# Kernel optimization log

Measured on AMD Instinct MI355X. Metric: run time of the kernel, lower is better.

The kernel has to match this reference:

```python
import jax, jax.numpy as jnp
import numpy as np
import math

N, M, S, D = 256, 512, 128, 512  # num_vids, num_music, num_segments, embed_dim


def layer_norm(x, g, b, eps=1e-5):
    mu = jnp.mean(x, axis=-1, keepdims=True)
    var = jnp.mean(jnp.square(x - mu), axis=-1, keepdims=True)
    return (x - mu) * jax.lax.rsqrt(var + eps) * g + b


def setup_inputs() -> dict:
    key = jax.random.key(0)
    ks = jax.random.split(key, 16)
    s = 0.02
    return {
        "video_embeds": jax.random.normal(ks[0], (N, D), jnp.float32),
        "music_embeds": jax.random.normal(ks[1], (M, S, D), jnp.float32),
        "music_mask": jnp.ones((M, S), jnp.int32),
        "ln1_g": jnp.ones((D,), jnp.float32), "ln1_b": jnp.zeros((D,), jnp.float32),
        "Wq": jax.random.normal(ks[2], (D, D), jnp.float32) * s, "bq": jnp.zeros((D,), jnp.float32),
        "Wk": jax.random.normal(ks[3], (D, D), jnp.float32) * s, "bk": jnp.zeros((D,), jnp.float32),
        "Wv": jax.random.normal(ks[4], (D, D), jnp.float32) * s, "bv": jnp.zeros((D,), jnp.float32),
        "Wo": jax.random.normal(ks[5], (D, D), jnp.float32) * s, "bo": jnp.zeros((D,), jnp.float32),
        "Wl": jax.random.normal(ks[6], (D, D), jnp.float32) * s, "bl": jnp.zeros((D,), jnp.float32),
        "ln2_g": jnp.ones((D,), jnp.float32), "ln2_b": jnp.zeros((D,), jnp.float32),
        "ln3_g": jnp.ones((D,), jnp.float32), "ln3_b": jnp.zeros((D,), jnp.float32),
    }


def reference(video_embeds, music_embeds, music_mask,
              ln1_g, ln1_b, Wq, bq, Wk, bk, Wv, bv, Wo, bo, Wl, bl,
              ln2_g, ln2_b, ln3_g, ln3_b):
    d = video_embeds.shape[-1]
    # layer_norm1 applied to both streams
    v_ln = layer_norm(video_embeds, ln1_g, ln1_b)           # (N, D)
    m_ln = layer_norm(music_embeds, ln1_g, ln1_b)           # (M, S, D)
    # single-head cross-attention (MultiHeadedAttention_mask, num_heads=1)
    q = v_ln @ Wq.T + bq                                    # (N, D)
    k = m_ln @ Wk.T + bk                                    # (M, S, D)
    v = m_ln @ Wv.T + bv                                    # (M, S, D)
    logits = jnp.einsum('nd,msd->mns', q, k) / math.sqrt(d)  # (M, N, S)
    logits = jnp.where(music_mask[:, None, :] == 0, -jnp.inf, logits)
    weights = jax.nn.softmax(logits, axis=-1)               # softmax over segments
    attn = jnp.einsum('mns,msd->mnd', weights, v)           # (M, N, D)
    o = attn @ Wo.T + bo                                    # (M, N, D)
    # layer_norm2 -> linear -> residual (dropout is identity in eval) -> layer_norm3
    o = layer_norm(o, ln2_g, ln2_b)
    lin = o @ Wl.T + bl
    out = layer_norm(o + lin, ln3_g, ln3_b)
    return out
```

## Files before the change

### kernel.cpp

```cpp
#include <hip/hip_runtime.h>

typedef __attribute__((ext_vector_type(8))) short short8;
typedef __attribute__((ext_vector_type(4))) float f32x4;
typedef __attribute__((ext_vector_type(4))) unsigned short u16x4;

__device__ __forceinline__ unsigned short f2bf(float f){
  unsigned int u = __builtin_bit_cast(unsigned int, f);
  u = (u + 0x7FFFu + ((u >> 16) & 1u)) >> 16;
  return (unsigned short)u;
}
__device__ __forceinline__ float bf2f(unsigned short h){
  unsigned int u = ((unsigned int)h) << 16;
  return __builtin_bit_cast(float, u);
}
__device__ __forceinline__ f32x4 mfma16(short8 a, short8 b, f32x4 c){
  return __builtin_amdgcn_mfma_f32_16x16x32_bf16(a, b, c, 0, 0, 0);
}
__device__ __forceinline__ void gload16(const void* g, void* l){
  __builtin_amdgcn_global_load_lds((const __attribute__((address_space(1))) void*)g,
                                   (__attribute__((address_space(3))) void*)l, 16, 0, 0);
}

__global__ __launch_bounds__(256) void cvt2_f32_bf16(const float* __restrict__ s0,
                                                     unsigned short* __restrict__ d0,
                                                     const float* __restrict__ s1,
                                                     unsigned short* __restrict__ d1){
  const int half = blockIdx.x >> 8;
  const float* src = half ? s1 : s0;
  unsigned short* dst = half ? d1 : d0;
  int i = ((blockIdx.x & 255) * 256 + threadIdx.x) * 4;
  float4 v = *(const float4*)(src + i);
  u16x4 o = { f2bf(v.x), f2bf(v.y), f2bf(v.z), f2bf(v.w) };
  *(u16x4*)(dst + i) = o;
}

__global__ __launch_bounds__(256) void copy_bf(const unsigned short* __restrict__ src,
                                               unsigned short* __restrict__ dst){
  int i = (blockIdx.x * 256 + threadIdx.x) * 8;
  *(short8*)(dst + i) = *(const short8*)(src + i);
}

__global__ __launch_bounds__(256) void ln_rows(const float* __restrict__ x,
                                               const float* __restrict__ g,
                                               const float* __restrict__ b,
                                               unsigned short* __restrict__ y,
                                               int nrows){
  const int wid = threadIdx.x >> 6, lane = threadIdx.x & 63;
  const int row = blockIdx.x * 4 + wid;
  if (row >= nrows) return;
  const float* xr = x + (long)row * 512;
  float4 v0 = *(const float4*)(xr + lane * 4);
  float4 v1 = *(const float4*)(xr + 256 + lane * 4);
  float s  = v0.x + v0.y + v0.z + v0.w + v1.x + v1.y + v1.z + v1.w;
  float s2 = v0.x*v0.x + v0.y*v0.y + v0.z*v0.z + v0.w*v0.w
           + v1.x*v1.x + v1.y*v1.y + v1.z*v1.z + v1.w*v1.w;
  #pragma unroll
  for (int m = 1; m < 64; m <<= 1){ s += __shfl_xor(s, m); s2 += __shfl_xor(s2, m); }
  const float mu = s * (1.f/512.f);
  const float rstd = rsqrtf(s2 * (1.f/512.f) - mu*mu + 1e-5f);
  float4 g0 = *(const float4*)(g + lane*4), g1 = *(const float4*)(g + 256 + lane*4);
  float4 b0 = *(const float4*)(b + lane*4), b1 = *(const float4*)(b + 256 + lane*4);
  u16x4 o0 = { f2bf((v0.x-mu)*rstd*g0.x + b0.x), f2bf((v0.y-mu)*rstd*g0.y + b0.y),
               f2bf((v0.z-mu)*rstd*g0.z + b0.z), f2bf((v0.w-mu)*rstd*g0.w + b0.w) };
  u16x4 o1 = { f2bf((v1.x-mu)*rstd*g1.x + b1.x), f2bf((v1.y-mu)*rstd*g1.y + b1.y),
               f2bf((v1.z-mu)*rstd*g1.z + b1.z), f2bf((v1.w-mu)*rstd*g1.w + b1.w) };
  *(u16x4*)(y + (long)row * 512 + lane * 4) = o0;
  *(u16x4*)(y + (long)row * 512 + 256 + lane * 4) = o1;
}

__global__ __launch_bounds__(256) void ln_weight_prep(
    const float* __restrict__ Wl, const float* __restrict__ g2,
    const float* __restrict__ b2, const float* __restrict__ bl,
    const float* __restrict__ bo,
    unsigned short* __restrict__ wlp, float* __restrict__ u,
    float* __restrict__ v, float* __restrict__ bias_cat){
  const int wid = threadIdx.x >> 6, lane = threadIdx.x & 63;
  const int n = blockIdx.x * 4 + wid;
  const float* row = Wl + (long)n * 512;
  float su = 0.f, sv = 0.f, sc = 0.f;
  #pragma unroll
  for (int h = 0; h < 2; ++h){
    const int c0 = h * 256 + lane * 4;
    float4 w  = *(const float4*)(row + c0);
    float4 gg = *(const float4*)(g2 + c0);
    float4 bb = *(const float4*)(b2 + c0);
    float4 oo = *(const float4*)(bo + c0);
    float4 wp = { w.x*gg.x, w.y*gg.y, w.z*gg.z, w.w*gg.w };
    su += wp.x + wp.y + wp.z + wp.w;
    sv += w.x*bb.x + w.y*bb.y + w.z*bb.z + w.w*bb.w;
    sc += wp.x*oo.x + wp.y*oo.y + wp.z*oo.z + wp.w*oo.w;
    u16x4 o = { f2bf(wp.x), f2bf(wp.y), f2bf(wp.z), f2bf(wp.w) };
    *(u16x4*)(wlp + (long)n * 512 + c0) = o;
  }
  #pragma unroll
  for (int m = 1; m < 64; m <<= 1){
    su += __shfl_xor(su, m); sv += __shfl_xor(sv, m); sc += __shfl_xor(sc, m);
  }
  if (lane == 0){
    u[n] = su;
    v[n] = sv + bl[n];
    bias_cat[n] = bo[n];
    bias_cat[512 + n] = sc;
  }
}

__global__ __launch_bounds__(256) void cvb_add(const unsigned short* __restrict__ Bc,
                                               const float* __restrict__ bv,
                                               float* __restrict__ bias_cat){
  const int wid = threadIdx.x >> 6, lane = threadIdx.x & 63;
  const int n = blockIdx.x * 4 + wid;
  const unsigned short* row = Bc + (long)n * 512;
  short8 a = *(const short8*)(row + lane * 8);
  float s = 0.f;
  #pragma unroll
  for (int j = 0; j < 8; ++j) s += bf2f((unsigned short)a[j]) * bv[lane*8 + j];
  #pragma unroll
  for (int m = 1; m < 64; m <<= 1) s += __shfl_xor(s, m);
  if (lane == 0) bias_cat[n] += s;
}

__global__ __launch_bounds__(256) void transpose3_bf(
    const float* __restrict__ s0, unsigned short* __restrict__ d0,
    const float* __restrict__ s1, unsigned short* __restrict__ d1,
    const float* __restrict__ s2, unsigned short* __restrict__ d2){
  __shared__ float tile[64][65];
  const float* src = (blockIdx.z == 0) ? s0 : (blockIdx.z == 1) ? s1 : s2;
  unsigned short* dst = (blockIdx.z == 0) ? d0 : (blockIdx.z == 1) ? d1 : d2;
  const int t = threadIdx.x;
  const int k0 = blockIdx.x * 64, c0 = blockIdx.y * 64;
  const int j = t & 63, i = t >> 6;
  #pragma unroll
  for (int rr = 0; rr < 16; ++rr)
    tile[i + rr*4][j] = src[(long)(c0 + i + rr*4) * 512 + k0 + j];
  __syncthreads();
  #pragma unroll
  for (int rr = 0; rr < 16; ++rr)
    dst[(long)(k0 + i + rr*4) * 512 + c0 + j] = f2bf(tile[j][i + rr*4]);
}

__global__ __launch_bounds__(256) void gemm_bt(const unsigned short* __restrict__ A,
                                               const unsigned short* __restrict__ B,
                                               const float* __restrict__ bias,
                                               unsigned short* __restrict__ out,
                                               int transposed){
  __shared__ unsigned short At[128][40];
  __shared__ unsigned short Bt[128][40];
  const int t = threadIdx.x, lane = t & 63, wid = t >> 6;
  const int l15 = lane & 15, l4 = lane >> 4;
  const int wr = wid >> 1, wc = wid & 1;
  const int rowBase = blockIdx.y * 128;
  const int colBase = blockIdx.x * 128;
  f32x4 zero = {0.f, 0.f, 0.f, 0.f};
  f32x4 acc[4][4];
  #pragma unroll
  for (int i = 0; i < 4; ++i)
    #pragma unroll
    for (int j = 0; j < 4; ++j) acc[i][j] = zero;
  const int sr = t >> 1, sh = (t & 1) * 16;
  for (int ks = 0; ks < 16; ++ks){
    const int k0 = ks * 32;
    const unsigned short* sa = A + (long)(rowBase + sr) * 512 + k0 + sh;
    *(short8*)&At[sr][sh]     = *(const short8*)sa;
    *(short8*)&At[sr][sh + 8] = *(const short8*)(sa + 8);
    const unsigned short* sb = B + (long)(colBase + sr) * 512 + k0 + sh;
    *(short8*)&Bt[sr][sh]     = *(const short8*)sb;
    *(short8*)&Bt[sr][sh + 8] = *(const short8*)(sb + 8);
    __syncthreads();
    short8 af[4], bfv[4];
    #pragma unroll
    for (int i = 0; i < 4; ++i) af[i]  = *(const short8*)&At[wr*64 + i*16 + l15][l4*8];
    #pragma unroll
    for (int i = 0; i < 4; ++i) bfv[i] = *(const short8*)&Bt[wc*64 + i*16 + l15][l4*8];
    #pragma unroll
    for (int i = 0; i < 4; ++i)
      #pragma unroll
      for (int j = 0; j < 4; ++j)
        acc[i][j] = mfma16(af[i], bfv[j], acc[i][j]);
    __syncthreads();
  }
  #pragma unroll
  for (int i = 0; i < 4; ++i){
    const int r0 = rowBase + wr*64 + i*16 + l4*4;
    #pragma unroll
    for (int j = 0; j < 4; ++j){
      const int c = colBase + wc*64 + j*16 + l15;
      const float bb = bias ? bias[c] : 0.f;
      #pragma unroll
      for (int jr = 0; jr < 4; ++jr){
        const float v = acc[i][j][jr] + bb;
        const long rr = r0 + jr;
        if (!transposed){
          out[rr * 512 + c] = f2bf(v);
        } else {
          const long m = rr >> 7, s = rr & 127;
          out[(m * 512 + c) * 128 + s] = f2bf(v);
        }
      }
    }
  }
}

__global__ __launch_bounds__(256) void vb97(const unsigned short* __restrict__ A,
                                            const unsigned short* __restrict__ B,
                                            unsigned short* __restrict__ vbt,
                                            int m0){
  __shared__ unsigned short A_lds[8192];
  __shared__ unsigned short B_lds[8192];
  const int t = threadIdx.x, lane = t & 63, wid = t >> 6;
  const int l15 = lane & 15, l4 = lane >> 4;
  const int wr = wid >> 1, wc = wid & 1;
  const int b = blockIdx.x;
  const int kk = b >> 3;
  const int colBase = (kk & 7) * 128;
  const long panel = m0 + (b & 7) + 8 * (kk >> 3);
  const long rowBase = panel * 128;
  f32x4 zero = {0.f,0.f,0.f,0.f};
  f32x4 acc[4][4];
  #pragma unroll
  for (int i = 0; i < 4; ++i)
    #pragma unroll
    for (int j = 0; j < 4; ++j) acc[i][j] = zero;
  for (int ks = 0; ks < 8; ++ks){
    const int k0 = ks * 64;
    #pragma unroll
    for (int sub = 0; sub < 2; ++sub){
      #pragma unroll
      for (int h = 0; h < 2; ++h){
        const int p = h*256 + t;
        const int row = p >> 2, g = (p & 3) ^ ((row >> 1) & 3);
        gload16(A + (rowBase + row)*512 + k0 + sub*32 + g*8, A_lds + sub*4096 + p*8);
        gload16(B + (long)(colBase + row)*512 + k0 + sub*32 + g*8, B_lds + sub*4096 + p*8);
      }
    }
    __syncthreads();
    #pragma unroll
    for (int sub = 0; sub < 2; ++sub){
      short8 af[4], bfv[4];
      #pragma unroll
      for (int i = 0; i < 4; ++i){
        const int ra = wr*64 + i*16 + l15;
        af[i]  = *(const short8*)(A_lds + sub*4096 + (ra*4 + (l4 ^ ((ra >> 1) & 3)))*8);
        const int rb = wc*64 + i*16 + l15;
        bfv[i] = *(const short8*)(B_lds + sub*4096 + (rb*4 + (l4 ^ ((rb >> 1) & 3)))*8);
      }
      #pragma unroll
      for (int i = 0; i < 4; ++i)
        #pragma unroll
        for (int j = 0; j < 4; ++j)
          acc[i][j] = mfma16(af[i], bfv[j], acc[i][j]);
    }
    __syncthreads();
  }
  #pragma unroll
  for (int i = 0; i < 4; ++i){
    const int s0 = wr*64 + i*16 + l4*4;
    #pragma unroll
    for (int j = 0; j < 4; ++j){
      const int n = colBase + wc*64 + j*16 + l15;
      #pragma unroll
      for (int jr = 0; jr < 4; ++jr)
        vbt[((long)panel*1024 + n)*128 + s0 + jr] = f2bf(acc[i][j][jr]);
    }
  }
}

__global__ __launch_bounds__(256) void attn_c(const unsigned short* __restrict__ q2,
                                              const unsigned short* __restrict__ mlnb,
                                              int m_mln0,
                                              const unsigned short* __restrict__ vbt,
                                              const int* __restrict__ mask,
                                              unsigned short* __restrict__ C,
                                              int m0){
  __shared__ __align__(16) char smem[81920];
  unsigned short* q_lin = (unsigned short*)smem;
  unsigned short* k_lin = (unsigned short*)(smem + 65536);
  unsigned short (*w_lds)[136] = (unsigned short (*)[136])smem;
  float* red = (float*)(smem + 17408);
  unsigned short* v_lin = (unsigned short*)(smem + 19456);
  const int b = blockIdx.x;
  const int m_local = (b & 7) + 8 * (b >> 5);
  const int qb = (b >> 3) & 3;
  const int m = m0 + m_local;
  const int t = threadIdx.x, lane = t & 63, wid = t >> 6;
  const int l15 = lane & 15, l4 = lane >> 4;
  #pragma unroll
  for (int it = 0; it < 16; ++it){
    const int p = it*256 + t;
    const int row = p >> 6, gp = p & 63;
    const int gsrc = gp ^ (row & 7);
    gload16(q2 + (long)(qb*64 + row)*512 + gsrc*8, q_lin + p*8);
  }
  f32x4 zero = {0.f,0.f,0.f,0.f};
  f32x4 acc[4][2];
  #pragma unroll
  for (int i = 0; i < 4; ++i){ acc[i][0] = zero; acc[i][1] = zero; }
  const unsigned short* kbase = mlnb + (long)(m - m_mln0) * 128 * 512;
  for (int ks = 0; ks < 8; ++ks){
    const int k0 = ks * 64;
    #pragma unroll
    for (int sub = 0; sub < 2; ++sub){
      #pragma unroll
      for (int h = 0; h < 2; ++h){
        const int p = h*256 + t;
        const int row = p >> 2, g = (p & 3) ^ ((row >> 1) & 3);
        gload16(kbase + (long)row*512 + k0 + sub*32 + g*8, k_lin + sub*4096 + p*8);
      }
    }
    __syncthreads();
    #pragma unroll
    for (int sub = 0; sub < 2; ++sub){
      const int kk32 = ks*2 + sub;
      short8 af[4], bfv[2];
      #pragma unroll
      for (int i = 0; i < 4; ++i){
        const int row = i*16 + l15;
        const int gp = (kk32*4 + l4) ^ (l15 & 7);
        af[i] = *(const short8*)(q_lin + (row*64 + gp)*8);
      }
      #pragma unroll
      for (int j = 0; j < 2; ++j){
        const int rb = wid*32 + j*16 + l15;
        bfv[j] = *(const short8*)(k_lin + sub*4096 + (rb*4 + (l4 ^ ((rb >> 1) & 3)))*8);
      }
      #pragma unroll
      for (int i = 0; i < 4; ++i)
        #pragma unroll
        for (int j = 0; j < 2; ++j)
          acc[i][j] = mfma16(af[i], bfv[j], acc[i][j]);
    }
    __syncthreads();
  }
  const float scale = 0.04419417382415922f;
  const int* mrow = mask + m * 128;
  const int mk0 = mrow[wid*32 + l15];
  const int mk1 = mrow[wid*32 + 16 + l15];
  float e[4][2][4], wmax[4][4], wsum[4][4];
  #pragma unroll
  for (int i = 0; i < 4; ++i)
    #pragma unroll
    for (int jr = 0; jr < 4; ++jr){
      float v0 = mk0 ? acc[i][0][jr]*scale : -3.0e38f;
      float v1 = mk1 ? acc[i][1][jr]*scale : -3.0e38f;
      float mx = fmaxf(v0, v1);
      mx = fmaxf(mx, __shfl_xor(mx, 1));
      mx = fmaxf(mx, __shfl_xor(mx, 2));
      mx = fmaxf(mx, __shfl_xor(mx, 4));
      mx = fmaxf(mx, __shfl_xor(mx, 8));
      const float e0 = __expf(v0 - mx), e1 = __expf(v1 - mx);
      float sm = e0 + e1;
      sm += __shfl_xor(sm, 1);
      sm += __shfl_xor(sm, 2);
      sm += __shfl_xor(sm, 4);
      sm += __shfl_xor(sm, 8);
      e[i][0][jr] = e0; e[i][1][jr] = e1;
      wmax[i][jr] = mx; wsum[i][jr] = sm;
    }
  if (l15 == 0){
    #pragma unroll
    for (int i = 0; i < 4; ++i)
      #pragma unroll
      for (int jr = 0; jr < 4; ++jr){
        const int r = i*16 + l4*4 + jr;
        red[r*8 + wid*2]     = wmax[i][jr];
        red[r*8 + wid*2 + 1] = wsum[i][jr];
      }
  }
  __syncthreads();
  #pragma unroll
  for (int i = 0; i < 4; ++i)
    #pragma unroll
    for (int jr = 0; jr < 4; ++jr){
      const int r = i*16 + l4*4 + jr;
      float4 a = *(const float4*)(red + r*8);
      float4 c = *(const float4*)(red + r*8 + 4);
      const float gm = fmaxf(fmaxf(a.x, a.z), fmaxf(c.x, c.z));
      const float gs = a.y*__expf(a.x - gm) + a.w*__expf(a.z - gm)
                     + c.y*__expf(c.x - gm) + c.w*__expf(c.z - gm);
      const float inv = (gs > 0.f) ? (1.f / gs) : 0.f;
      const float sc = __expf(wmax[i][jr] - gm) * inv;
      #pragma unroll
      for (int j = 0; j < 2; ++j)
        w_lds[r][wid*32 + j*16 + l15] = f2bf(e[i][j][jr] * sc);
    }
  const long rowb = (long)m * 256 + qb * 64;
  const unsigned short* vbase = vbt + (long)m * 1024 * 128;
  for (int nb = 0; nb < 8; ++nb){
    __syncthreads();
    #pragma unroll
    for (int it = 0; it < 8; ++it){
      const int p = it*256 + t;
      const int row = p >> 4, g = (p & 15) ^ (row & 7);
      gload16(vbase + (long)(nb*128 + row)*128 + g*8, v_lin + p*8);
    }
    __syncthreads();
    f32x4 pacc[4][2];
    #pragma unroll
    for (int i = 0; i < 4; ++i){ pacc[i][0] = zero; pacc[i][1] = zero; }
    #pragma unroll
    for (int ks2 = 0; ks2 < 4; ++ks2){
      short8 wf[4], vf[2];
      #pragma unroll
      for (int i = 0; i < 4; ++i) wf[i] = *(const short8*)&w_lds[i*16 + l15][ks2*32 + l4*8];
      #pragma unroll
      for (int j = 0; j < 2; ++j){
        const int rv = wid*32 + j*16 + l15;
        vf[j] = *(const short8*)(v_lin + (rv*16 + ((ks2*4 + l4) ^ (rv & 7)))*8);
      }
      #pragma unroll
      for (int i = 0; i < 4; ++i)
        #pragma unroll
        for (int j = 0; j < 2; ++j)
          pacc[i][j] = mfma16(wf[i], vf[j], pacc[i][j]);
    }
    #pragma unroll
    for (int i = 0; i < 4; ++i)
      #pragma unroll
      for (int j = 0; j < 2; ++j)
        #pragma unroll
        for (int jr = 0; jr < 4; ++jr)
          C[(rowb + i*16 + l4*4 + jr) * 1024 + nb*128 + wid*32 + j*16 + l15] =
              f2bf(pacc[i][j][jr]);
  }
}

__global__ __launch_bounds__(256) void ln_epilogue(
    const unsigned short* Cb, float* out,
    const float* __restrict__ bias_cat, const float* __restrict__ u,
    const float* __restrict__ v,
    const float* __restrict__ g2, const float* __restrict__ b2,
    const float* __restrict__ g3, const float* __restrict__ b3){
  const int wid = threadIdx.x >> 6, lane = threadIdx.x & 63;
  const long row = (long)blockIdx.x * 4 + wid;
  const unsigned short* cr = Cb + row * 1024;
  short8 ov = *(const short8*)(cr + lane * 8);
  short8 pv = *(const short8*)(cr + 512 + lane * 8);
  const int n0 = lane * 8;
  float4 bo0 = *(const float4*)(bias_cat + n0);
  float4 bo1 = *(const float4*)(bias_cat + n0 + 4);
  float4 c20 = *(const float4*)(bias_cat + 512 + n0);
  float4 c21 = *(const float4*)(bias_cat + 512 + n0 + 4);
  float o[8], p[8];
  #pragma unroll
  for (int j = 0; j < 4; ++j){
    o[j]   = bf2f((unsigned short)ov[j])   + ((const float*)&bo0)[j];
    o[4+j] = bf2f((unsigned short)ov[4+j]) + ((const float*)&bo1)[j];
    p[j]   = bf2f((unsigned short)pv[j])   + ((const float*)&c20)[j];
    p[4+j] = bf2f((unsigned short)pv[4+j]) + ((const float*)&c21)[j];
  }
  float s = 0.f, s2 = 0.f;
  #pragma unroll
  for (int j = 0; j < 8; ++j){ s += o[j]; s2 += o[j]*o[j]; }
  #pragma unroll
  for (int m = 1; m < 64; m <<= 1){ s += __shfl_xor(s, m); s2 += __shfl_xor(s2, m); }
  const float mu2 = s * (1.f/512.f);
  const float rstd2 = rsqrtf(s2 * (1.f/512.f) - mu2*mu2 + 1e-5f);
  float4 uv0 = *(const float4*)(u + n0), uv1 = *(const float4*)(u + n0 + 4);
  float4 vv0 = *(const float4*)(v + n0), vv1 = *(const float4*)(v + n0 + 4);
  float4 g20v = *(const float4*)(g2 + n0), g21v = *(const float4*)(g2 + n0 + 4);
  float4 b20v = *(const float4*)(b2 + n0), b21v = *(const float4*)(b2 + n0 + 4);
  float y[8];
  #pragma unroll
  for (int j = 0; j < 4; ++j){
    const float lin0 = rstd2 * (p[j]   - mu2 * ((const float*)&uv0)[j]) + ((const float*)&vv0)[j];
    const float lin1 = rstd2 * (p[4+j] - mu2 * ((const float*)&uv1)[j]) + ((const float*)&vv1)[j];
    const float oln0 = (o[j]   - mu2) * rstd2 * ((const float*)&g20v)[j] + ((const float*)&b20v)[j];
    const float oln1 = (o[4+j] - mu2) * rstd2 * ((const float*)&g21v)[j] + ((const float*)&b21v)[j];
    y[j]   = oln0 + lin0;
    y[4+j] = oln1 + lin1;
  }
  float t1 = 0.f, t2 = 0.f;
  #pragma unroll
  for (int j = 0; j < 8; ++j){ t1 += y[j]; t2 += y[j]*y[j]; }
  #pragma unroll
  for (int m = 1; m < 64; m <<= 1){ t1 += __shfl_xor(t1, m); t2 += __shfl_xor(t2, m); }
  const float mu3 = t1 * (1.f/512.f);
  const float rstd3 = rsqrtf(t2 * (1.f/512.f) - mu3*mu3 + 1e-5f);
  float4 g30v = *(const float4*)(g3 + n0), g31v = *(const float4*)(g3 + n0 + 4);
  float4 b30v = *(const float4*)(b3 + n0), b31v = *(const float4*)(b3 + n0 + 4);
  float4 r0, r1;
  #pragma unroll
  for (int j = 0; j < 4; ++j){
    ((float*)&r0)[j] = (y[j]   - mu3) * rstd3 * ((const float*)&g30v)[j] + ((const float*)&b30v)[j];
    ((float*)&r1)[j] = (y[4+j] - mu3) * rstd3 * ((const float*)&g31v)[j] + ((const float*)&b31v)[j];
  }
  *(float4*)(out + row * 512 + n0)     = r0;
  *(float4*)(out + row * 512 + n0 + 4) = r1;
}

extern "C" void kernel_launch(void* const* d_in, const int* in_sizes, int n_in,
                              void* d_out, int out_size, void* d_ws, size_t ws_size,
                              hipStream_t stream){
  const float* video = (const float*)d_in[0];
  const float* music = (const float*)d_in[1];
  const int*   mask  = (const int*)d_in[2];
  const float* ln1g  = (const float*)d_in[3];
  const float* ln1b  = (const float*)d_in[4];
  const float* Wq = (const float*)d_in[5];  const float* bq = (const float*)d_in[6];
  const float* Wk = (const float*)d_in[7];
  const float* Wv = (const float*)d_in[9];  const float* bv = (const float*)d_in[10];
  const float* Wo = (const float*)d_in[11]; const float* bo = (const float*)d_in[12];
  const float* Wl = (const float*)d_in[13]; const float* bl = (const float*)d_in[14];
  const float* g2 = (const float*)d_in[15]; const float* b2 = (const float*)d_in[16];
  const float* g3 = (const float*)d_in[17]; const float* b3 = (const float*)d_in[18];

  char* ob = (char*)d_out;
  unsigned short* mln  = (unsigned short*)(ob + 201326592);
  unsigned short* Cb   = (unsigned short*)ob;
  float* outp = (float*)d_out;

  char* wsb = (char*)d_ws;
  unsigned short* vbt    = (unsigned short*)wsb;
  unsigned short* Wq_bf  = (unsigned short*)(wsb + 134217728);
  unsigned short* Bcat   = Wq_bf + 262144;
  unsigned short* wlp    = Bcat + 524288;
  unsigned short* WoT    = wlp + 262144;
  unsigned short* WkT    = WoT + 262144;
  unsigned short* WvT    = WkT + 262144;
  unsigned short* Wvb    = WvT + 262144;
  unsigned short* q_ws   = Wvb + 524288;
  unsigned short* q2_ws  = q_ws + 131072;
  unsigned short* vln    = q2_ws + 131072;
  unsigned short* mln_cp = vln + 131072;
  float* bias_cat = (float*)(mln_cp + 524288);
  float* u_vec    = bias_cat + 1024;
  float* v_vec    = u_vec + 512;

  cvt2_f32_bf16<<<512, 256, 0, stream>>>(Wq, Wq_bf, Wo, Bcat);
  ln_weight_prep<<<128, 256, 0, stream>>>(Wl, g2, b2, bl, bo, wlp, u_vec, v_vec, bias_cat);
  transpose3_bf<<<dim3(8, 8, 3), 256, 0, stream>>>(Wo, WoT, Wk, WkT, Wv, WvT);
  gemm_bt<<<dim3(4, 4), 256, 0, stream>>>(wlp, WoT, nullptr, Bcat + 262144, 0);
  gemm_bt<<<dim3(4, 8), 256, 0, stream>>>(Bcat, WvT, nullptr, Wvb, 0);
  cvb_add<<<256, 256, 0, stream>>>(Bcat, bv, bias_cat);

  ln_rows<<<16384, 256, 0, stream>>>(music, ln1g, ln1b, mln, 65536);
  ln_rows<<<64,    256, 0, stream>>>(video, ln1g, ln1b, vln, 256);
  gemm_bt<<<dim3(4, 2), 256, 0, stream>>>(vln, Wq_bf, bq, q_ws, 0);
  gemm_bt<<<dim3(4, 2), 256, 0, stream>>>(q_ws, WkT, nullptr, q2_ws, 0);

  const int vm0[5] = {0, 128, 256, 384, 480};
  const int vdm[5] = {128, 128, 128, 96, 32};
  const int am0[5] = {0, 128, 256, 384, 480};
  const int adm[5] = {128, 128, 128, 96, 24};
  for (int cidx = 0; cidx < 5; ++cidx){
    vb97<<<vdm[cidx] * 8, 256, 0, stream>>>(mln, Wvb, vbt, vm0[cidx]);
    const int m0 = am0[cidx], dm = adm[cidx];
    attn_c<<<dm * 4, 256, 0, stream>>>(q2_ws, mln, 0, vbt, mask, Cb, m0);
    ln_epilogue<<<dm * 64, 256, 0, stream>>>(Cb + (long)m0*256*1024,
                                             outp + (long)m0*256*512,
                                             bias_cat, u_vec, v_vec, g2, b2, g3, b3);
  }
  copy_bf<<<256, 256, 0, stream>>>(mln + (long)504*128*512, mln_cp);
  attn_c<<<32, 256, 0, stream>>>(q2_ws, mln_cp, 504, vbt, mask, Cb, 504);
  ln_epilogue<<<512, 256, 0, stream>>>(Cb + (long)504*256*1024,
                                       outp + (long)504*256*512,
                                       bias_cat, u_vec, v_vec, g2, b2, g3, b3);
}
```

Measured before the change: 598.5 us.

## Double-buffer K and V LDS tiles in attention kernel and swizzle weight tile

```diff
diff --git a/kernel.cpp b/kernel.cpp
--- a/kernel.cpp
+++ b/kernel.cpp
@@ -273,10 +273,12 @@
                                               int m0){
   __shared__ __align__(16) char smem[81920];
   unsigned short* q_lin = (unsigned short*)smem;
-  unsigned short* k_lin = (unsigned short*)(smem + 65536);
-  unsigned short (*w_lds)[136] = (unsigned short (*)[136])smem;
-  float* red = (float*)(smem + 17408);
-  unsigned short* v_lin = (unsigned short*)(smem + 19456);
+  unsigned short* k_half0 = (unsigned short*)(smem + 65536);
+  unsigned short* k_half1 = (unsigned short*)(smem + 73728);
+  unsigned short* w_lds = (unsigned short*)smem;
+  unsigned short* v_half0 = (unsigned short*)(smem + 16384);
+  unsigned short* v_half1 = (unsigned short*)(smem + 49152);
+  float* red = (float*)(smem + 49152);
   const int b = blockIdx.x;
   const int m_local = (b & 7) + 8 * (b >> 5);
   const int qb = (b >> 3) & 3;
@@ -295,46 +297,47 @@
   #pragma unroll
   for (int i = 0; i < 4; ++i){ acc[i][0] = zero; acc[i][1] = zero; }
   const unsigned short* kbase = mlnb + (long)(m - m_mln0) * 128 * 512;
-  for (int ks = 0; ks < 8; ++ks){
-    const int k0 = ks * 64;
-    #pragma unroll
-    for (int sub = 0; sub < 2; ++sub){
-      #pragma unroll
-      for (int h = 0; h < 2; ++h){
-        const int p = h*256 + t;
-        const int row = p >> 2, g = (p & 3) ^ ((row >> 1) & 3);
-        gload16(kbase + (long)row*512 + k0 + sub*32 + g*8, k_lin + sub*4096 + p*8);
-      }
-    }
+  #define STAGE_K(ksub, dst)                                                  \
+    do {                                                                      \
+      _Pragma("unroll")                                                       \
+      for (int h2 = 0; h2 < 2; ++h2){                                         \
+        const int p = h2*256 + t;                                             \
+        const int row = p >> 2, g = (p & 3) ^ ((row >> 1) & 3);               \
+        gload16(kbase + (long)row*512 + (ksub)*32 + g*8, (dst) + p*8);        \
+      }                                                                       \
+    } while (0)
+  STAGE_K(0, k_half0);
+  for (int ks = 0; ks < 16; ++ks){
     __syncthreads();
-    #pragma unroll
-    for (int sub = 0; sub < 2; ++sub){
-      const int kk32 = ks*2 + sub;
-      short8 af[4], bfv[2];
-      #pragma unroll
-      for (int i = 0; i < 4; ++i){
-        const int row = i*16 + l15;
-        const int gp = (kk32*4 + l4) ^ (l15 & 7);
-        af[i] = *(const short8*)(q_lin + (row*64 + gp)*8);
-      }
-      #pragma unroll
-      for (int j = 0; j < 2; ++j){
-        const int rb = wid*32 + j*16 + l15;
-        bfv[j] = *(const short8*)(k_lin + sub*4096 + (rb*4 + (l4 ^ ((rb >> 1) & 3)))*8);
-      }
-      #pragma unroll
-      for (int i = 0; i < 4; ++i)
-        #pragma unroll
-        for (int j = 0; j < 2; ++j)
-          acc[i][j] = mfma16(af[i], bfv[j], acc[i][j]);
-    }
-    __syncthreads();
-  }
+    if (ks < 15){
+      if (ks & 1){ STAGE_K(ks + 1, k_half0); } else { STAGE_K(ks + 1, k_half1); }
+    }
+    const unsigned short* kh = (ks & 1) ? k_half1 : k_half0;
+    short8 af[4], bfv[2];
+    #pragma unroll
+    for (int i = 0; i < 4; ++i){
+      const int row = i*16 + l15;
+      const int gp = (ks*4 + l4) ^ (l15 & 7);
+      af[i] = *(const short8*)(q_lin + (row*64 + gp)*8);
+    }
+    #pragma unroll
+    for (int j = 0; j < 2; ++j){
+      const int rb = wid*32 + j*16 + l15;
+      bfv[j] = *(const short8*)(kh + (rb*4 + (l4 ^ ((rb >> 1) & 3)))*8);
+    }
+    #pragma unroll
+    for (int i = 0; i < 4; ++i)
+      #pragma unroll
+      for (int j = 0; j < 2; ++j)
+        acc[i][j] = mfma16(af[i], bfv[j], acc[i][j]);
+  }
+  #undef STAGE_K
+  __syncthreads();
   const float scale = 0.04419417382415922f;
   const int* mrow = mask + m * 128;
   const int mk0 = mrow[wid*32 + l15];
   const int mk1 = mrow[wid*32 + 16 + l15];
-  float e[4][2][4], wmax[4][4], wsum[4][4];
+  float e[4][2][4], wmax[4][4];
   #pragma unroll
   for (int i = 0; i < 4; ++i)
     #pragma unroll
@@ -353,18 +356,13 @@
       sm += __shfl_xor(sm, 4);
       sm += __shfl_xor(sm, 8);
       e[i][0][jr] = e0; e[i][1][jr] = e1;
-      wmax[i][jr] = mx; wsum[i][jr] = sm;
-    }
-  if (l15 == 0){
-    #pragma unroll
-    for (int i = 0; i < 4; ++i)
-      #pragma unroll
-      for (int jr = 0; jr < 4; ++jr){
+      wmax[i][jr] = mx;
+      if (l15 == 0){
         const int r = i*16 + l4*4 + jr;
-        red[r*8 + wid*2]     = wmax[i][jr];
-        red[r*8 + wid*2 + 1] = wsum[i][jr];
-      }
-  }
+        red[r*8 + wid*2]     = mx;
+        red[r*8 + wid*2 + 1] = sm;
+      }
+    }
   __syncthreads();
   #pragma unroll
   for (int i = 0; i < 4; ++i)
@@ -379,20 +377,29 @@
       const float inv = (gs > 0.f) ? (1.f / gs) : 0.f;
       const float sc = __expf(wmax[i][jr] - gm) * inv;
       #pragma unroll
-      for (int j = 0; j < 2; ++j)
-        w_lds[r][wid*32 + j*16 + l15] = f2bf(e[i][j][jr] * sc);
+      for (int j = 0; j < 2; ++j){
+        const int cc = wid*32 + j*16 + l15;
+        w_lds[r*128 + (((cc >> 3) ^ (r & 7)) << 3) + (cc & 7)] = f2bf(e[i][j][jr] * sc);
+      }
     }
   const long rowb = (long)m * 256 + qb * 64;
   const unsigned short* vbase = vbt + (long)m * 1024 * 128;
+  #define STAGE_V(nb, dst)                                                    \
+    do {                                                                      \
+      _Pragma("unroll")                                                       \
+      for (int it = 0; it < 8; ++it){                                         \
+        const int p = it*256 + t;                                             \
+        const int row = p >> 4, g = (p & 15) ^ (row & 7);                     \
+        gload16(vbase + (long)((nb)*128 + row)*128 + g*8, (dst) + p*8);       \
+      }                                                                       \
+    } while (0)
+  STAGE_V(0, v_half0);
   for (int nb = 0; nb < 8; ++nb){
     __syncthreads();
-    #pragma unroll
-    for (int it = 0; it < 8; ++it){
-      const int p = it*256 + t;
-      const int row = p >> 4, g = (p & 15) ^ (row & 7);
-      gload16(vbase + (long)(nb*128 + row)*128 + g*8, v_lin + p*8);
-    }
-    __syncthreads();
+    if (nb < 7){
+      if (nb & 1){ STAGE_V(nb + 1, v_half0); } else { STAGE_V(nb + 1, v_half1); }
+    }
+    const unsigned short* vh = (nb & 1) ? v_half1 : v_half0;
     f32x4 pacc[4][2];
     #pragma unroll
     for (int i = 0; i < 4; ++i){ pacc[i][0] = zero; pacc[i][1] = zero; }
@@ -400,11 +407,15 @@
     for (int ks2 = 0; ks2 < 4; ++ks2){
       short8 wf[4], vf[2];
       #pragma unroll
-      for (int i = 0; i < 4; ++i) wf[i] = *(const short8*)&w_lds[i*16 + l15][ks2*32 + l4*8];
+      for (int i = 0; i < 4; ++i){
+        const int row = i*16 + l15;
+        const int gsw = (ks2*4 + l4) ^ (row & 7);
+        wf[i] = *(const short8*)(w_lds + row*128 + gsw*8);
+      }
       #pragma unroll
       for (int j = 0; j < 2; ++j){
         const int rv = wid*32 + j*16 + l15;
-        vf[j] = *(const short8*)(v_lin + (rv*16 + ((ks2*4 + l4) ^ (rv & 7)))*8);
+        vf[j] = *(const short8*)(vh + (rv*16 + ((ks2*4 + l4) ^ (rv & 7)))*8);
       }
       #pragma unroll
       for (int i = 0; i < 4; ++i)
@@ -421,6 +432,7 @@
           C[(rowb + i*16 + l4*4 + jr) * 1024 + nb*128 + wid*32 + j*16 + l15] =
               f2bf(pacc[i][j][jr]);
   }
+  #undef STAGE_V
 }
 
 __global__ __launch_bounds__(256) void ln_epilogue(
```

Result: no change. 587.8 us (median of 2 runs) (-1.8%).
